# Kernel optimization log

Measured on AMD Instinct MI355X. Metric: run time of the kernel, lower is better.

Reference implementation:

```python
import jax, jax.numpy as jnp
import numpy as np

B, C, H, W = 4, 256, 64, 64
HEADS, GROUPS = 8, 8
HEAD_DIM = C // HEADS
EPS_GN = 1e-5
EPS_NORM = 1e-12


def group_norm(x, gamma, beta):
    b, c, h, w = x.shape
    xr = x.reshape(b, GROUPS, c // GROUPS, h, w)
    mean = xr.mean(axis=(2, 3, 4), keepdims=True)
    var = xr.var(axis=(2, 3, 4), keepdims=True)
    xn = ((xr - mean) / jnp.sqrt(var + EPS_GN)).reshape(b, c, h, w)
    return xn * gamma[None, :, None, None] + beta[None, :, None, None]


def conv1x1(x, w):
    # w: (C_out, C_in) pointwise conv
    return jnp.einsum('oc,bchw->bohw', w, x)


def dwconv3x3(x, w, b):
    # depthwise 3x3, w: (C, 1, 3, 3)
    y = jax.lax.conv_general_dilated(
        x, w, window_strides=(1, 1), padding='SAME',
        dimension_numbers=('NCHW', 'OIHW', 'NCHW'),
        feature_group_count=C)
    return y + b[None, :, None, None]


def setup_inputs() -> dict:
    key = jax.random.key(0)
    ks = jax.random.split(key, 7)
    s = 0.05
    f32 = jnp.float32
    return {
        'x': jax.random.normal(ks[0], (B, C, H, W), f32),
        'wq': jax.random.normal(ks[1], (C, C), f32) * s,
        'gq_gamma': jnp.ones((C,), f32), 'gq_beta': jnp.zeros((C,), f32),
        'wk': jax.random.normal(ks[2], (C, C), f32) * s,
        'gk_gamma': jnp.ones((C,), f32), 'gk_beta': jnp.zeros((C,), f32),
        'wv': jax.random.normal(ks[3], (C, C), f32) * s,
        'wp': jax.random.normal(ks[4], (C, C), f32) * s,
        'bp': jnp.zeros((C,), f32),
        'gp_gamma': jnp.ones((C,), f32), 'gp_beta': jnp.zeros((C,), f32),
        'dw1': jax.random.normal(ks[5], (C, 1, 3, 3), f32) * s,
        'db1': jnp.zeros((C,), f32),
        'dw2': jax.random.normal(ks[6], (C, 1, 3, 3), f32) * s,
        'db2': jnp.zeros((C,), f32),
    }


def reference(x, wq, gq_gamma, gq_beta, wk, gk_gamma, gk_beta, wv,
              wp, bp, gp_gamma, gp_beta, dw1, db1, dw2, db2):
    b, c, h, w = x.shape
    q = group_norm(conv1x1(x, wq), gq_gamma, gq_beta)
    k = group_norm(conv1x1(x, wk), gk_gamma, gk_beta)
    v = conv1x1(x, wv)

    def to_tokens(t):
        # (B,C,H,W) -> (B*H*W, heads, head_dim)
        return t.transpose(0, 2, 3, 1).reshape(b * h * w, HEADS, HEAD_DIM)

    q, k, v = to_tokens(q), to_tokens(k), to_tokens(v)
    qn = q / jnp.maximum(jnp.linalg.norm(q, axis=-1, keepdims=True), EPS_NORM)
    kn = k / jnp.maximum(jnp.linalg.norm(k, axis=-1, keepdims=True), EPS_NORM)
    scale = 1.0 / np.sqrt(HEAD_DIM).astype(np.float32)
    # per-pixel spectral attention: (N, heads, d, d)
    attn = jnp.einsum('nhd,nhe->nhde', qn, kn) * scale
    attn = jax.nn.softmax(attn, axis=-1)
    out = jnp.einsum('nhde,nhe->nhd', attn, v)
    out = out.reshape(b, h, w, c).transpose(0, 3, 1, 2)

    pos = dwconv3x3(x, dw1, db1)
    pos = jax.nn.gelu(pos, approximate=False)
    pos = dwconv3x3(pos, dw2, db2)

    out = out + pos
    out = conv1x1(out, wp) + bp[None, :, None, None]
    out = group_norm(out, gp_gamma, gp_beta)
    return out
```

## Files before the change

### kernel.cpp

```cpp
#include <hip/hip_runtime.h>
#include <math.h>
#include <stdint.h>

#define C_ 256
#define HW_ 4096
#define PLANE (C_*HW_)
#define INV_CNT (1.f / 131072.f)
#define NSLOT 16

typedef __attribute__((ext_vector_type(8))) short bf16x8;
typedef __attribute__((ext_vector_type(4))) float f32x4;

__device__ __forceinline__ unsigned short f2bf(float f) {
    union { float f; unsigned int u; } v; v.f = f;
    unsigned int r = v.u + 0x7fffu + ((v.u >> 16) & 1u);
    return (unsigned short)(r >> 16);
}

__device__ __forceinline__ float bf2f(unsigned short u) {
    return __uint_as_float(((unsigned)u) << 16);
}

__device__ __forceinline__ void load_lds16(const void* g, void* l) {
    __builtin_amdgcn_global_load_lds(
        (const __attribute__((address_space(1))) unsigned int*)g,
        (__attribute__((address_space(3))) unsigned int*)l, 16, 0, 0);
}

__global__ __launch_bounds__(256) void transpose_cvt_kernel(
    const float* __restrict__ src, unsigned short* __restrict__ dst,
    const float* __restrict__ wq, const float* __restrict__ wk,
    const float* __restrict__ wv, const float* __restrict__ wp,
    unsigned short* __restrict__ wbf, float* __restrict__ stats)
{
    __shared__ float tile[64][65];
    int t = threadIdx.x;

    int bid = blockIdx.x + 64 * (blockIdx.y + 4 * blockIdx.z);
    {
        int widx = bid * 256 + t;
        const float* s = (widx < 65536) ? wq : (widx < 131072) ? wk
                       : (widx < 196608) ? wv : wp;
        wbf[widx] = f2bf(s[widx & 65535]);
        if (bid == 0) {
#pragma unroll
            for (int i = 0; i < 12; i++) stats[t + i * 256] = 0.f;
        }
    }

    int b = blockIdx.z;
    const float* s = src + (size_t)b * PLANE;
    unsigned short* d = dst + (size_t)b * PLANE;
    int c0 = blockIdx.y * 64, n0 = blockIdx.x * 64;
    int r = t >> 6, col = t & 63;
#pragma unroll
    for (int i = 0; i < 16; i++)
        tile[r + i * 4][col] = s[(size_t)(c0 + r + i * 4) * HW_ + n0 + col];
    __syncthreads();
#pragma unroll
    for (int i = 0; i < 16; i++)
        d[(size_t)(n0 + r + i * 4) * 256 + c0 + col] = f2bf(tile[col][r + i * 4]);
}

__global__ __launch_bounds__(256) void transpose_cvt_add_kernel(
    const unsigned short* __restrict__ pos, const unsigned short* __restrict__ attn,
    unsigned short* __restrict__ dst)
{
    __shared__ float tile[64][65];
    int b = blockIdx.z;
    const unsigned short* s = pos + (size_t)b * PLANE;
    const unsigned short* a = attn + (size_t)b * PLANE;
    unsigned short* d = dst + (size_t)b * PLANE;
    int c0 = blockIdx.y * 64, n0 = blockIdx.x * 64;
    int t = threadIdx.x;
    int r = t >> 6, col = t & 63;
#pragma unroll
    for (int i = 0; i < 16; i++)
        tile[r + i * 4][col] = bf2f(s[(size_t)(c0 + r + i * 4) * HW_ + n0 + col]);
    __syncthreads();
#pragma unroll
    for (int i = 0; i < 16; i++) {
        size_t o = (size_t)(n0 + r + i * 4) * 256 + c0 + col;
        d[o] = f2bf(tile[col][r + i * 4] + bf2f(a[o]));
    }
}

__device__ __forceinline__ void mfma_core(
    const unsigned short* __restrict__ A,
    const unsigned short* __restrict__ Bm,
    int m0, int n0, f32x4 (&acc)[4][4])
{
    __shared__ unsigned short As[2][128 * 32];
    __shared__ unsigned short Bs[2][128 * 32];
    const int t = threadIdx.x;
    const int lane = t & 63, wave = t >> 6;

#pragma unroll
    for (int i = 0; i < 4; i++)
#pragma unroll
        for (int j = 0; j < 4; j++) acc[i][j] = (f32x4)0.f;

    const int srow = wave * 32 + (lane >> 2);
    const int scol = (lane & 3) * 8;
    const unsigned short* ga = A  + (size_t)(m0 + srow) * 256 + scol;
    const unsigned short* gb = Bm + (size_t)(n0 + srow) * 256 + scol;
    const int lbase = (wave * 32) * 32;

    const int wm = wave >> 1, wn = wave & 1;
    const int fr = lane & 15, kg = lane >> 4;

    for (int k0 = 0; k0 < 256; k0 += 64) {
        if (k0) __syncthreads();
        load_lds16(ga + k0,            As[0] + lbase);
        load_lds16(ga + k0 + 16 * 256, As[0] + lbase + 16 * 32);
        load_lds16(gb + k0,            Bs[0] + lbase);
        load_lds16(gb + k0 + 16 * 256, Bs[0] + lbase + 16 * 32);
        load_lds16(ga + k0 + 32,            As[1] + lbase);
        load_lds16(ga + k0 + 32 + 16 * 256, As[1] + lbase + 16 * 32);
        load_lds16(gb + k0 + 32,            Bs[1] + lbase);
        load_lds16(gb + k0 + 32 + 16 * 256, Bs[1] + lbase + 16 * 32);
        __syncthreads();

#pragma unroll
        for (int kk = 0; kk < 2; kk++) {
            bf16x8 af[4], bfr[4];
#pragma unroll
            for (int i = 0; i < 4; i++) {
                af[i]  = *(const bf16x8*)(As[kk] + (wm * 64 + i * 16 + fr) * 32 + kg * 8);
                bfr[i] = *(const bf16x8*)(Bs[kk] + (wn * 64 + i * 16 + fr) * 32 + kg * 8);
            }
#pragma unroll
            for (int mi = 0; mi < 4; mi++)
#pragma unroll
                for (int ni = 0; ni < 4; ni++)
                    acc[mi][ni] = __builtin_amdgcn_mfma_f32_16x16x32_bf16(
                        af[mi], bfr[ni], acc[mi][ni], 0, 0, 0);
        }
    }
}

__device__ __forceinline__ void stat_atomic(
    float s0, float ss0, float s1, float ss1, float* d0, float* d1)
{
#pragma unroll
    for (int off = 32; off >= 1; off >>= 1) {
        s0  += __shfl_down(s0, off);  ss0 += __shfl_down(ss0, off);
        s1  += __shfl_down(s1, off);  ss1 += __shfl_down(ss1, off);
    }
    if ((threadIdx.x & 63) == 0) {
        atomicAdd(d0, s0); atomicAdd(d0 + 1, ss0);
        atomicAdd(d1, s1); atomicAdd(d1 + 1, ss1);
    }
}

__device__ __forceinline__ void stat_read(const float* sp, float& S, float& SS) {
    S = 0.f; SS = 0.f;
#pragma unroll
    for (int i = 0; i < NSLOT; i++) { S += sp[i * 2]; SS += sp[i * 2 + 1]; }
}

__global__ __launch_bounds__(256) void gemm_qkv_mfma(
    const unsigned short* __restrict__ wbf, const unsigned short* __restrict__ xT,
    unsigned short* __restrict__ q, unsigned short* __restrict__ k,
    unsigned short* __restrict__ v, float* __restrict__ stats)
{
    int z = blockIdx.z;
    int batch = z & 3, which = z >> 2;
    unsigned short* Y = ((which == 0) ? q : (which == 1) ? k : v)
                        + (size_t)batch * PLANE;
    const unsigned short* A  = wbf + which * 65536;
    const unsigned short* Bm = xT + (size_t)batch * PLANE;
    const int m0 = blockIdx.x * 128;
    const int n0 = blockIdx.y * 128;

    f32x4 acc[4][4];
    mfma_core(A, Bm, m0, n0, acc);

    const int lane = threadIdx.x & 63, wave = threadIdx.x >> 6;
    const int wm = wave >> 1, wn = wave & 1;
    const int cl = lane & 15, qd = lane >> 4;

    if (which < 2) {
        float s[2] = {0.f, 0.f}, ss[2] = {0.f, 0.f};
#pragma unroll
        for (int mi = 0; mi < 4; mi++)
#pragma unroll
            for (int ni = 0; ni < 4; ni++)
#pragma unroll
                for (int r = 0; r < 4; r++) {
                    float vv = acc[mi][ni][r];
                    s[mi >> 1] += vv; ss[mi >> 1] += vv * vv;
                }
        int g0 = (m0 >> 5) + wm * 2;
        int slot = blockIdx.y & (NSLOT - 1);
        float* d0 = stats + (size_t)(which * 32 + batch * 8 + g0) * (NSLOT * 2) + slot * 2;
        stat_atomic(s[0], ss[0], s[1], ss[1], d0, d0 + NSLOT * 2);
    }

#pragma unroll
    for (int mi = 0; mi < 4; mi++) {
        int oc = m0 + wm * 64 + mi * 16 + qd * 4;
#pragma unroll
        for (int ni = 0; ni < 4; ni++) {
            int token = n0 + wn * 64 + ni * 16 + cl;
            uint2 pk;
            pk.x = (unsigned)f2bf(acc[mi][ni][0]) | ((unsigned)f2bf(acc[mi][ni][1]) << 16);
            pk.y = (unsigned)f2bf(acc[mi][ni][2]) | ((unsigned)f2bf(acc[mi][ni][3]) << 16);
            *(uint2*)&Y[(size_t)token * 256 + oc] = pk;
        }
    }
}

__global__ __launch_bounds__(256) void gemm_out_mfma(
    const unsigned short* __restrict__ wbf, const unsigned short* __restrict__ aT,
    const float* __restrict__ bp, float* __restrict__ y, float* __restrict__ stats)
{
    int batch = blockIdx.z;
    const unsigned short* A  = aT + (size_t)batch * PLANE;
    const unsigned short* Bm = wbf + 3 * 65536;
    float* Y = y + (size_t)batch * PLANE;
    const int m0 = blockIdx.x * 128;
    const int n0 = blockIdx.y * 128;

    f32x4 acc[4][4];
    mfma_core(A, Bm, m0, n0, acc);

    const int lane = threadIdx.x & 63, wave = threadIdx.x >> 6;
    const int wm = wave >> 1, wn = wave & 1;
    const int cl = lane & 15, qd = lane >> 4;

    float s[2] = {0.f, 0.f}, ss[2] = {0.f, 0.f};
#pragma unroll
    for (int ni = 0; ni < 4; ni++) {
        int oc = n0 + wn * 64 + ni * 16 + cl;
        float bb = bp[oc];
#pragma unroll
        for (int mi = 0; mi < 4; mi++) {
            int tk = m0 + wm * 64 + mi * 16 + qd * 4;
            float4 o;
            o.x = acc[mi][ni][0] + bb; o.y = acc[mi][ni][1] + bb;
            o.z = acc[mi][ni][2] + bb; o.w = acc[mi][ni][3] + bb;
            s[ni >> 1] += o.x + o.y + o.z + o.w;
            ss[ni >> 1] += o.x * o.x + o.y * o.y + o.z * o.z + o.w * o.w;
            *(float4*)&Y[(size_t)oc * HW_ + tk] = o;
        }
    }
    int g0 = (n0 >> 5) + wn * 2;
    int slot = blockIdx.x & (NSLOT - 1);
    float* d0 = stats + (size_t)(64 + batch * 8 + g0) * (NSLOT * 2) + slot * 2;
    stat_atomic(s[0], ss[0], s[1], ss[1], d0, d0 + NSLOT * 2);
}

__device__ __forceinline__ void bf16x32_load(const unsigned short* p, float* o) {
    const uint4* u4 = (const uint4*)p;
#pragma unroll
    for (int i = 0; i < 4; i++) {
        uint4 u = u4[i];
        o[i*8+0] = __uint_as_float(u.x << 16); o[i*8+1] = __uint_as_float(u.x & 0xffff0000u);
        o[i*8+2] = __uint_as_float(u.y << 16); o[i*8+3] = __uint_as_float(u.y & 0xffff0000u);
        o[i*8+4] = __uint_as_float(u.z << 16); o[i*8+5] = __uint_as_float(u.z & 0xffff0000u);
        o[i*8+6] = __uint_as_float(u.w << 16); o[i*8+7] = __uint_as_float(u.w & 0xffff0000u);
    }
}

__global__ __launch_bounds__(256) void attn_tok_kernel(
    const unsigned short* __restrict__ qtok, const unsigned short* __restrict__ ktok,
    const unsigned short* __restrict__ vtok, const float* __restrict__ stats,
    const float* __restrict__ gqg, const float* __restrict__ gqb,
    const float* __restrict__ gkg, const float* __restrict__ gkb,
    unsigned short* __restrict__ out)
{
    __shared__ float sqg[256], sqb[256], skg[256], skb[256];
    const int t = threadIdx.x;
    sqg[t] = gqg[t]; sqb[t] = gqb[t]; skg[t] = gkg[t]; skb[t] = gkb[t];
    __syncthreads();

    const int h = t & 7;
    const int pix = blockIdx.x * 32 + (t >> 3);
    const int b = pix >> 12;
    const size_t base = (size_t)pix * 256 + h * 32;
    const float K2 = 0.17677669529663687f * 1.4426950408889634f;

    float a[32], kn[32], vv[32];

    {
        float S, SS;
        stat_read(stats + (size_t)(b * 8 + h) * (NSLOT * 2), S, SS);
        float m = S * INV_CNT;
        float r = rsqrtf(SS * INV_CNT - m * m + 1e-5f);
        float qv[32], ssum = 0.f;
        bf16x32_load(qtok + base, qv);
#pragma unroll
        for (int j = 0; j < 32; j++) {
            float g = r * sqg[h * 32 + j];
            qv[j] = (qv[j] - m) * g + sqb[h * 32 + j];
            ssum = fmaf(qv[j], qv[j], ssum);
        }
        float inv = K2 / fmaxf(sqrtf(ssum), 1e-12f);
#pragma unroll
        for (int j = 0; j < 32; j++) a[j] = qv[j] * inv;
    }
    {
        float S, SS;
        stat_read(stats + (size_t)(32 + b * 8 + h) * (NSLOT * 2), S, SS);
        float m = S * INV_CNT;
        float r = rsqrtf(SS * INV_CNT - m * m + 1e-5f);
        float ssum = 0.f;
        bf16x32_load(ktok + base, kn);
#pragma unroll
        for (int j = 0; j < 32; j++) {
            float g = r * skg[h * 32 + j];
            kn[j] = (kn[j] - m) * g + skb[h * 32 + j];
            ssum = fmaf(kn[j], kn[j], ssum);
        }
        float inv = 1.f / fmaxf(sqrtf(ssum), 1e-12f);
#pragma unroll
        for (int j = 0; j < 32; j++) kn[j] *= inv;
    }
    bf16x32_load(vtok + base, vv);

    uint4* op = (uint4*)(out + base);
#pragma unroll
    for (int di = 0; di < 4; di++) {
        unsigned int od[4];
#pragma unroll
        for (int dp = 0; dp < 4; dp++) {
            float o2[2];
#pragma unroll
            for (int dd = 0; dd < 2; dd++) {
                float ad = a[di * 8 + dp * 2 + dd];
                float num = 0.f, den = 0.f;
#pragma unroll
                for (int e = 0; e < 32; e++) {
                    float w = __builtin_amdgcn_exp2f(ad * kn[e]);
                    num = fmaf(w, vv[e], num);
                    den += w;
                }
                o2[dd] = num / den;
            }
            od[dp] = (unsigned)f2bf(o2[0]) | ((unsigned)f2bf(o2[1]) << 16);
        }
        op[di] = make_uint4(od[0], od[1], od[2], od[3]);
    }
}

__device__ __forceinline__ float gelu_exact(float v) {
    return 0.5f * v * (1.f + erff(v * 0.70710678118654752f));
}

__global__ __launch_bounds__(256) void dwconv_fused_kernel(
    const float* __restrict__ x,
    const float* __restrict__ dw1, const float* __restrict__ db1,
    const float* __restrict__ dw2, const float* __restrict__ db2,
    unsigned short* __restrict__ pos)
{
    __shared__ float xs[66 * 68];
    __shared__ float ps[66 * 68];
    const int bc = blockIdx.x;
    const int c = bc & 255;
    const int t = threadIdx.x;
    const float* plane = x + (size_t)bc * 4096;

    float w1[9], w2[9];
#pragma unroll
    for (int i = 0; i < 9; i++) { w1[i] = dw1[c * 9 + i]; w2[i] = dw2[c * 9 + i]; }
    const float b1 = db1[c], b2 = db2[c];

    for (int i = t; i < 66 * 66; i += 256) {
        int r = i / 66, cc = i - r * 66;
        int gr = r - 1, gc = cc - 1;
        float v = 0.f;
        if ((unsigned)gr < 64u && (unsigned)gc < 64u) v = plane[gr * 64 + gc];
        xs[r * 68 + cc] = v;
    }
    __syncthreads();

    for (int i = t; i < 66 * 66; i += 256) {
        int pr = i / 66, pc = i - pr * 66;
        int gr = pr - 1, gc = pc - 1;
        float val = 0.f;
        if ((unsigned)gr < 64u && (unsigned)gc < 64u) {
            float s = b1;
#pragma unroll
            for (int ky = 0; ky < 3; ky++)
#pragma unroll
                for (int kx = 0; kx < 3; kx++)
                    s += w1[ky * 3 + kx] * xs[(gr + ky) * 68 + (gc + kx)];
            val = gelu_exact(s);
        }
        ps[pr * 68 + pc] = val;
    }
    __syncthreads();

    for (int i = t; i < 4096; i += 256) {
        int orow = i >> 6, ocol = i & 63;
        float s = b2;
#pragma unroll
        for (int ky = 0; ky < 3; ky++)
#pragma unroll
            for (int kx = 0; kx < 3; kx++)
                s += w2[ky * 3 + kx] * ps[(orow + ky) * 68 + (ocol + kx)];
        pos[(size_t)bc * 4096 + i] = f2bf(s);
    }
}

__global__ __launch_bounds__(256) void gn_apply_kernel(
    float* __restrict__ y, const float* __restrict__ stats,
    const float* __restrict__ gamma, const float* __restrict__ beta)
{
    int i4 = blockIdx.x * 256 + threadIdx.x;
    int idx = i4 * 4;
    int c = (idx >> 12) & 255;
    int bg = ((idx >> 20) << 3) | (c >> 5);
    float S, SS;
    stat_read(stats + (size_t)(64 + bg) * (NSLOT * 2), S, SS);
    float mean = S * INV_CNT;
    float rstd = rsqrtf(SS * INV_CNT - mean * mean + 1e-5f);
    float ga = rstd * gamma[c], be = beta[c] - mean * ga;
    float4 v4 = *(float4*)&y[idx];
    v4.x = v4.x * ga + be;
    v4.y = v4.y * ga + be;
    v4.z = v4.z * ga + be;
    v4.w = v4.w * ga + be;
    *(float4*)&y[idx] = v4;
}

extern "C" void kernel_launch(void* const* d_in, const int* in_sizes, int n_in,
                              void* d_out, int out_size, void* d_ws, size_t ws_size,
                              hipStream_t stream)
{
    const float* x   = (const float*)d_in[0];
    const float* wq  = (const float*)d_in[1];
    const float* gqg = (const float*)d_in[2];
    const float* gqb = (const float*)d_in[3];
    const float* wk  = (const float*)d_in[4];
    const float* gkg = (const float*)d_in[5];
    const float* gkb = (const float*)d_in[6];
    const float* wv  = (const float*)d_in[7];
    const float* wp  = (const float*)d_in[8];
    const float* bp  = (const float*)d_in[9];
    const float* gpg = (const float*)d_in[10];
    const float* gpb = (const float*)d_in[11];
    const float* dw1 = (const float*)d_in[12];
    const float* db1 = (const float*)d_in[13];
    const float* dw2 = (const float*)d_in[14];
    const float* db2 = (const float*)d_in[15];
    float* out = (float*)d_out;

    char* ws = (char*)d_ws;
    const size_t MB8 = (size_t)8 * 1024 * 1024;
    unsigned short* qtok = (unsigned short*)(ws);
    unsigned short* ktok = (unsigned short*)(ws + MB8);
    unsigned short* vtok = (unsigned short*)(ws + 2 * MB8);
    unsigned short* atok = (unsigned short*)(ws + 3 * MB8);
    unsigned short* xT   = (unsigned short*)(ws + 4 * MB8);
    unsigned short* aT   = xT;
    unsigned short* pos  = qtok;
    unsigned short* wbf  = (unsigned short*)(ws + 5 * MB8);
    float*          stats= (float*)(ws + 5 * MB8 + 524288);

    dim3 blk(256);
    transpose_cvt_kernel<<<dim3(64, 4, 4), blk, 0, stream>>>(x, xT, wq, wk, wv, wp, wbf, stats);
    gemm_qkv_mfma<<<dim3(2, 32, 12), blk, 0, stream>>>(wbf, xT, qtok, ktok, vtok, stats);
    attn_tok_kernel<<<dim3(512), blk, 0, stream>>>(qtok, ktok, vtok, stats,
                                                   gqg, gqb, gkg, gkb, atok);
    dwconv_fused_kernel<<<dim3(1024), blk, 0, stream>>>(x, dw1, db1, dw2, db2, pos);
    transpose_cvt_add_kernel<<<dim3(64, 4, 4), blk, 0, stream>>>(pos, atok, aT);
    gemm_out_mfma<<<dim3(32, 2, 4), blk, 0, stream>>>(wbf, aT, bp, out, stats);
    gn_apply_kernel<<<dim3(4096), blk, 0, stream>>>(out, stats, gpg, gpb);
}
```

Baseline: 177.9 us.

## Merge depthwise conv into QKV GEMM launch and store pre-norm output as bf16

The QKV GEMM and the depthwise-conv/GELU branch now run as two block ranges of one launch that share a dynamically partitioned LDS buffer. This removes a launch and lets the memory-bound conv blocks overlap with the compute-bound GEMM blocks. Pos gets its own workspace region so it no longer aliases qtok. The output projection also writes a bf16 intermediate that gn_apply reads back, halving that round-trip traffic. The cost is extra rounding before the final group norm, and LDS use per block rises to the conv's size for the GEMM blocks too, which may lower occupancy.

```diff
diff --git a/kernel.cpp b/kernel.cpp
--- a/kernel.cpp
+++ b/kernel.cpp
@@ -88,10 +88,9 @@
 __device__ __forceinline__ void mfma_core(
     const unsigned short* __restrict__ A,
     const unsigned short* __restrict__ Bm,
-    int m0, int n0, f32x4 (&acc)[4][4])
-{
-    __shared__ unsigned short As[2][128 * 32];
-    __shared__ unsigned short Bs[2][128 * 32];
+    int m0, int n0, f32x4 (&acc)[4][4],
+    unsigned short* sA, unsigned short* sB)
+{
     const int t = threadIdx.x;
     const int lane = t & 63, wave = t >> 6;
 
@@ -111,14 +110,14 @@
 
     for (int k0 = 0; k0 < 256; k0 += 64) {
         if (k0) __syncthreads();
-        load_lds16(ga + k0,            As[0] + lbase);
-        load_lds16(ga + k0 + 16 * 256, As[0] + lbase + 16 * 32);
-        load_lds16(gb + k0,            Bs[0] + lbase);
-        load_lds16(gb + k0 + 16 * 256, Bs[0] + lbase + 16 * 32);
-        load_lds16(ga + k0 + 32,            As[1] + lbase);
-        load_lds16(ga + k0 + 32 + 16 * 256, As[1] + lbase + 16 * 32);
-        load_lds16(gb + k0 + 32,            Bs[1] + lbase);
-        load_lds16(gb + k0 + 32 + 16 * 256, Bs[1] + lbase + 16 * 32);
+        load_lds16(ga + k0,            sA + lbase);
+        load_lds16(ga + k0 + 16 * 256, sA + lbase + 16 * 32);
+        load_lds16(gb + k0,            sB + lbase);
+        load_lds16(gb + k0 + 16 * 256, sB + lbase + 16 * 32);
+        load_lds16(ga + k0 + 32,            sA + 4096 + lbase);
+        load_lds16(ga + k0 + 32 + 16 * 256, sA + 4096 + lbase + 16 * 32);
+        load_lds16(gb + k0 + 32,            sB + 4096 + lbase);
+        load_lds16(gb + k0 + 32 + 16 * 256, sB + 4096 + lbase + 16 * 32);
         __syncthreads();
 
 #pragma unroll
@@ -126,8 +125,8 @@
             bf16x8 af[4], bfr[4];
 #pragma unroll
             for (int i = 0; i < 4; i++) {
-                af[i]  = *(const bf16x8*)(As[kk] + (wm * 64 + i * 16 + fr) * 32 + kg * 8);
-                bfr[i] = *(const bf16x8*)(Bs[kk] + (wn * 64 + i * 16 + fr) * 32 + kg * 8);
+                af[i]  = *(const bf16x8*)(sA + kk * 4096 + (wm * 64 + i * 16 + fr) * 32 + kg * 8);
+                bfr[i] = *(const bf16x8*)(sB + kk * 4096 + (wn * 64 + i * 16 + fr) * 32 + kg * 8);
             }
 #pragma unroll
             for (int mi = 0; mi < 4; mi++)
@@ -159,71 +158,138 @@
     for (int i = 0; i < NSLOT; i++) { S += sp[i * 2]; SS += sp[i * 2 + 1]; }
 }
 
-__global__ __launch_bounds__(256) void gemm_qkv_mfma(
+__device__ __forceinline__ float gelu_exact(float v) {
+    return 0.5f * v * (1.f + erff(v * 0.70710678118654752f));
+}
+
+__global__ __launch_bounds__(256) void gemm_qkv_dw_kernel(
     const unsigned short* __restrict__ wbf, const unsigned short* __restrict__ xT,
     unsigned short* __restrict__ q, unsigned short* __restrict__ k,
-    unsigned short* __restrict__ v, float* __restrict__ stats)
-{
-    int z = blockIdx.z;
-    int batch = z & 3, which = z >> 2;
-    unsigned short* Y = ((which == 0) ? q : (which == 1) ? k : v)
-                        + (size_t)batch * PLANE;
-    const unsigned short* A  = wbf + which * 65536;
-    const unsigned short* Bm = xT + (size_t)batch * PLANE;
-    const int m0 = blockIdx.x * 128;
-    const int n0 = blockIdx.y * 128;
-
-    f32x4 acc[4][4];
-    mfma_core(A, Bm, m0, n0, acc);
-
-    const int lane = threadIdx.x & 63, wave = threadIdx.x >> 6;
-    const int wm = wave >> 1, wn = wave & 1;
-    const int cl = lane & 15, qd = lane >> 4;
-
-    if (which < 2) {
-        float s[2] = {0.f, 0.f}, ss[2] = {0.f, 0.f};
-#pragma unroll
-        for (int mi = 0; mi < 4; mi++)
-#pragma unroll
-            for (int ni = 0; ni < 4; ni++)
-#pragma unroll
-                for (int r = 0; r < 4; r++) {
-                    float vv = acc[mi][ni][r];
-                    s[mi >> 1] += vv; ss[mi >> 1] += vv * vv;
-                }
-        int g0 = (m0 >> 5) + wm * 2;
-        int slot = blockIdx.y & (NSLOT - 1);
-        float* d0 = stats + (size_t)(which * 32 + batch * 8 + g0) * (NSLOT * 2) + slot * 2;
-        stat_atomic(s[0], ss[0], s[1], ss[1], d0, d0 + NSLOT * 2);
-    }
-
-#pragma unroll
-    for (int mi = 0; mi < 4; mi++) {
-        int oc = m0 + wm * 64 + mi * 16 + qd * 4;
-#pragma unroll
-        for (int ni = 0; ni < 4; ni++) {
-            int token = n0 + wn * 64 + ni * 16 + cl;
-            uint2 pk;
-            pk.x = (unsigned)f2bf(acc[mi][ni][0]) | ((unsigned)f2bf(acc[mi][ni][1]) << 16);
-            pk.y = (unsigned)f2bf(acc[mi][ni][2]) | ((unsigned)f2bf(acc[mi][ni][3]) << 16);
-            *(uint2*)&Y[(size_t)token * 256 + oc] = pk;
+    unsigned short* __restrict__ v, float* __restrict__ stats,
+    const float* __restrict__ x,
+    const float* __restrict__ dw1, const float* __restrict__ db1,
+    const float* __restrict__ dw2, const float* __restrict__ db2,
+    unsigned short* __restrict__ pos)
+{
+    __shared__ __align__(16) char smem[66 * 68 * 4 * 2];
+    const int bid = blockIdx.x;
+    const int t = threadIdx.x;
+
+    if (bid < 768) {
+        unsigned short* sA = (unsigned short*)smem;
+        unsigned short* sB = (unsigned short*)(smem + 16384);
+        int z = bid >> 6, rr = bid & 63;
+        int batch = z & 3, which = z >> 2;
+        unsigned short* Y = ((which == 0) ? q : (which == 1) ? k : v)
+                            + (size_t)batch * PLANE;
+        const unsigned short* A  = wbf + which * 65536;
+        const unsigned short* Bm = xT + (size_t)batch * PLANE;
+        const int m0 = (rr & 1) * 128;
+        const int n0 = (rr >> 1) * 128;
+
+        f32x4 acc[4][4];
+        mfma_core(A, Bm, m0, n0, acc, sA, sB);
+
+        const int lane = t & 63, wave = t >> 6;
+        const int wm = wave >> 1, wn = wave & 1;
+        const int cl = lane & 15, qd = lane >> 4;
+
+        if (which < 2) {
+            float s[2] = {0.f, 0.f}, ss[2] = {0.f, 0.f};
+#pragma unroll
+            for (int mi = 0; mi < 4; mi++)
+#pragma unroll
+                for (int ni = 0; ni < 4; ni++)
+#pragma unroll
+                    for (int r = 0; r < 4; r++) {
+                        float vv = acc[mi][ni][r];
+                        s[mi >> 1] += vv; ss[mi >> 1] += vv * vv;
+                    }
+            int g0 = (m0 >> 5) + wm * 2;
+            int slot = (rr >> 1) & (NSLOT - 1);
+            float* d0 = stats + (size_t)(which * 32 + batch * 8 + g0) * (NSLOT * 2) + slot * 2;
+            stat_atomic(s[0], ss[0], s[1], ss[1], d0, d0 + NSLOT * 2);
+        }
+
+#pragma unroll
+        for (int mi = 0; mi < 4; mi++) {
+            int oc = m0 + wm * 64 + mi * 16 + qd * 4;
+#pragma unroll
+            for (int ni = 0; ni < 4; ni++) {
+                int token = n0 + wn * 64 + ni * 16 + cl;
+                uint2 pk;
+                pk.x = (unsigned)f2bf(acc[mi][ni][0]) | ((unsigned)f2bf(acc[mi][ni][1]) << 16);
+                pk.y = (unsigned)f2bf(acc[mi][ni][2]) | ((unsigned)f2bf(acc[mi][ni][3]) << 16);
+                *(uint2*)&Y[(size_t)token * 256 + oc] = pk;
+            }
+        }
+    } else {
+        float* xs = (float*)smem;
+        float* ps = xs + 66 * 68;
+        const int bc = bid - 768;
+        const int c = bc & 255;
+        const float* plane = x + (size_t)bc * 4096;
+
+        float w1[9], w2[9];
+#pragma unroll
+        for (int i = 0; i < 9; i++) { w1[i] = dw1[c * 9 + i]; w2[i] = dw2[c * 9 + i]; }
+        const float b1 = db1[c], b2 = db2[c];
+
+        for (int i = t; i < 66 * 66; i += 256) {
+            int r = i / 66, cc = i - r * 66;
+            int gr = r - 1, gc = cc - 1;
+            float vv = 0.f;
+            if ((unsigned)gr < 64u && (unsigned)gc < 64u) vv = plane[gr * 64 + gc];
+            xs[r * 68 + cc] = vv;
+        }
+        __syncthreads();
+
+        for (int i = t; i < 66 * 66; i += 256) {
+            int pr = i / 66, pc = i - pr * 66;
+            int gr = pr - 1, gc = pc - 1;
+            float val = 0.f;
+            if ((unsigned)gr < 64u && (unsigned)gc < 64u) {
+                float s = b1;
+#pragma unroll
+                for (int ky = 0; ky < 3; ky++)
+#pragma unroll
+                    for (int kx = 0; kx < 3; kx++)
+                        s += w1[ky * 3 + kx] * xs[(gr + ky) * 68 + (gc + kx)];
+                val = gelu_exact(s);
+            }
+            ps[pr * 68 + pc] = val;
+        }
+        __syncthreads();
+
+        for (int i = t; i < 4096; i += 256) {
+            int orow = i >> 6, ocol = i & 63;
+            float s = b2;
+#pragma unroll
+            for (int ky = 0; ky < 3; ky++)
+#pragma unroll
+                for (int kx = 0; kx < 3; kx++)
+                    s += w2[ky * 3 + kx] * ps[(orow + ky) * 68 + (ocol + kx)];
+            pos[(size_t)bc * 4096 + i] = f2bf(s);
         }
     }
 }
 
 __global__ __launch_bounds__(256) void gemm_out_mfma(
     const unsigned short* __restrict__ wbf, const unsigned short* __restrict__ aT,
-    const float* __restrict__ bp, float* __restrict__ y, float* __restrict__ stats)
-{
+    const float* __restrict__ bp, unsigned short* __restrict__ yb,
+    float* __restrict__ stats)
+{
+    __shared__ __align__(16) unsigned short sA[2 * 128 * 32];
+    __shared__ __align__(16) unsigned short sB[2 * 128 * 32];
     int batch = blockIdx.z;
     const unsigned short* A  = aT + (size_t)batch * PLANE;
     const unsigned short* Bm = wbf + 3 * 65536;
-    float* Y = y + (size_t)batch * PLANE;
+    unsigned short* Y = yb + (size_t)batch * PLANE;
     const int m0 = blockIdx.x * 128;
     const int n0 = blockIdx.y * 128;
 
     f32x4 acc[4][4];
-    mfma_core(A, Bm, m0, n0, acc);
+    mfma_core(A, Bm, m0, n0, acc, sA, sB);
 
     const int lane = threadIdx.x & 63, wave = threadIdx.x >> 6;
     const int wm = wave >> 1, wn = wave & 1;
@@ -242,7 +308,10 @@
             o.z = acc[mi][ni][2] + bb; o.w = acc[mi][ni][3] + bb;
             s[ni >> 1] += o.x + o.y + o.z + o.w;
             ss[ni >> 1] += o.x * o.x + o.y * o.y + o.z * o.z + o.w * o.w;
-            *(float4*)&Y[(size_t)oc * HW_ + tk] = o;
+            uint2 pk;
+            pk.x = (unsigned)f2bf(o.x) | ((unsigned)f2bf(o.y) << 16);
+            pk.y = (unsigned)f2bf(o.z) | ((unsigned)f2bf(o.w) << 16);
+            *(uint2*)&Y[(size_t)oc * HW_ + tk] = pk;
         }
     }
     int g0 = (n0 >> 5) + wn * 2;
@@ -344,68 +413,9 @@
     }
 }
 
-__device__ __forceinline__ float gelu_exact(float v) {
-    return 0.5f * v * (1.f + erff(v * 0.70710678118654752f));
-}
-
-__global__ __launch_bounds__(256) void dwconv_fused_kernel(
-    const float* __restrict__ x,
-    const float* __restrict__ dw1, const float* __restrict__ db1,
-    const float* __restrict__ dw2, const float* __restrict__ db2,
-    unsigned short* __restrict__ pos)
-{
-    __shared__ float xs[66 * 68];
-    __shared__ float ps[66 * 68];
-    const int bc = blockIdx.x;
-    const int c = bc & 255;
-    const int t = threadIdx.x;
-    const float* plane = x + (size_t)bc * 4096;
-
-    float w1[9], w2[9];
-#pragma unroll
-    for (int i = 0; i < 9; i++) { w1[i] = dw1[c * 9 + i]; w2[i] = dw2[c * 9 + i]; }
-    const float b1 = db1[c], b2 = db2[c];
-
-    for (int i = t; i < 66 * 66; i += 256) {
-        int r = i / 66, cc = i - r * 66;
-        int gr = r - 1, gc = cc - 1;
-        float v = 0.f;
-        if ((unsigned)gr < 64u && (unsigned)gc < 64u) v = plane[gr * 64 + gc];
-        xs[r * 68 + cc] = v;
-    }
-    __syncthreads();
-
-    for (int i = t; i < 66 * 66; i += 256) {
-        int pr = i / 66, pc = i - pr * 66;
-        int gr = pr - 1, gc = pc - 1;
-        float val = 0.f;
-        if ((unsigned)gr < 64u && (unsigned)gc < 64u) {
-            float s = b1;
-#pragma unroll
-            for (int ky = 0; ky < 3; ky++)
-#pragma unroll
-                for (int kx = 0; kx < 3; kx++)
-                    s += w1[ky * 3 + kx] * xs[(gr + ky) * 68 + (gc + kx)];
-            val = gelu_exact(s);
-        }
-        ps[pr * 68 + pc] = val;
-    }
-    __syncthreads();
-
-    for (int i = t; i < 4096; i += 256) {
-        int orow = i >> 6, ocol = i & 63;
-        float s = b2;
-#pragma unroll
-        for (int ky = 0; ky < 3; ky++)
-#pragma unroll
-            for (int kx = 0; kx < 3; kx++)
-                s += w2[ky * 3 + kx] * ps[(orow + ky) * 68 + (ocol + kx)];
-        pos[(size_t)bc * 4096 + i] = f2bf(s);
-    }
-}
-
 __global__ __launch_bounds__(256) void gn_apply_kernel(
-    float* __restrict__ y, const float* __restrict__ stats,
+    const unsigned short* __restrict__ src, float* __restrict__ y,
+    const float* __restrict__ stats,
     const float* __restrict__ gamma, const float* __restrict__ beta)
 {
     int i4 = blockIdx.x * 256 + threadIdx.x;
@@ -417,11 +427,12 @@
     float mean = S * INV_CNT;
     float rstd = rsqrtf(SS * INV_CNT - mean * mean + 1e-5f);
     float ga = rstd * gamma[c], be = beta[c] - mean * ga;
-    float4 v4 = *(float4*)&y[idx];
-    v4.x = v4.x * ga + be;
-    v4.y = v4.y * ga + be;
-    v4.z = v4.z * ga + be;
-    v4.w = v4.w * ga + be;
+    uint2 u = *(const uint2*)&src[idx];
+    float4 v4;
+    v4.x = bf2f((unsigned short)(u.x & 0xffff)) * ga + be;
+    v4.y = bf2f((unsigned short)(u.x >> 16))    * ga + be;
+    v4.z = bf2f((unsigned short)(u.y & 0xffff)) * ga + be;
+    v4.w = bf2f((unsigned short)(u.y >> 16))    * ga + be;
     *(float4*)&y[idx] = v4;
 }
 
@@ -455,17 +466,18 @@
     unsigned short* atok = (unsigned short*)(ws + 3 * MB8);
     unsigned short* xT   = (unsigned short*)(ws + 4 * MB8);
     unsigned short* aT   = xT;
-    unsigned short* pos  = qtok;
+    unsigned short* outb = ktok;
     unsigned short* wbf  = (unsigned short*)(ws + 5 * MB8);
     float*          stats= (float*)(ws + 5 * MB8 + 524288);
+    unsigned short* pos  = (unsigned short*)(ws + 6 * MB8);
 
     dim3 blk(256);
     transpose_cvt_kernel<<<dim3(64, 4, 4), blk, 0, stream>>>(x, xT, wq, wk, wv, wp, wbf, stats);
-    gemm_qkv_mfma<<<dim3(2, 32, 12), blk, 0, stream>>>(wbf, xT, qtok, ktok, vtok, stats);
+    gemm_qkv_dw_kernel<<<dim3(1792), blk, 0, stream>>>(wbf, xT, qtok, ktok, vtok, stats,
+                                                       x, dw1, db1, dw2, db2, pos);
     attn_tok_kernel<<<dim3(512), blk, 0, stream>>>(qtok, ktok, vtok, stats,
                                                    gqg, gqb, gkg, gkb, atok);
-    dwconv_fused_kernel<<<dim3(1024), blk, 0, stream>>>(x, dw1, db1, dw2, db2, pos);
     transpose_cvt_add_kernel<<<dim3(64, 4, 4), blk, 0, stream>>>(pos, atok, aT);
-    gemm_out_mfma<<<dim3(32, 2, 4), blk, 0, stream>>>(wbf, aT, bp, out, stats);
-    gn_apply_kernel<<<dim3(4096), blk, 0, stream>>>(out, stats, gpg, gpb);
-}
+    gemm_out_mfma<<<dim3(32, 2, 4), blk, 0, stream>>>(wbf, aT, bp, outb, stats);
+    gn_apply_kernel<<<dim3(4096), blk, 0, stream>>>(outb, out, stats, gpg, gpb);
+}
```

Result: slower. 182.0 us (+2.3%).
